# Kernel tuning notes

Measured on AMD Instinct MI355X. Metric: run time of the kernel, lower is better.

The kernel has to match this reference:

```python
import jax, jax.numpy as jnp
import numpy as np

OUT_FEATURES = 4096
IN_FEATURES = 4096
GROUP_SIZE = 256
NUM_GROUPS = OUT_FEATURES * IN_FEATURES // GROUP_SIZE  # 65536


def setup_inputs() -> dict:
    key = jax.random.key(0)
    k1, k2, k3 = jax.random.split(key, 3)
    x = jax.random.normal(k1, (4, 2048, IN_FEATURES), dtype=jnp.float32)
    weight_packed = jax.random.randint(k2, (NUM_GROUPS, GROUP_SIZE // 2), 0, 256, dtype=jnp.int32)
    # params[..., 0] = scale, params[..., 1] = zero_point; keep scales small like real quant params
    weight_params = jax.random.uniform(k3, (NUM_GROUPS, 2), dtype=jnp.float32) * jnp.array([0.01, 0.1], dtype=jnp.float32)
    return {"x": x, "weight_packed": weight_packed, "weight_params": weight_params}


def _dequantize_4bit(weight_packed, weight_params):
    # weight_packed: [G, gs/2] bytes, two 4-bit values per byte (low nibble = even index)
    scales = weight_params[:, 0:1]  # [G, 1]
    zeros = weight_params[:, 1:2]   # [G, 1]
    low = (weight_packed & 15).astype(jnp.float32)          # even positions
    high = ((weight_packed >> 4) & 15).astype(jnp.float32)  # odd positions
    q = jnp.stack([low, high], axis=-1).reshape(weight_packed.shape[0], -1)  # [G, gs]
    return q * scales + zeros


def reference(x, weight_packed, weight_params):
    w = _dequantize_4bit(weight_packed, weight_params)  # [G, gs]
    w = w.reshape(-1)[: OUT_FEATURES * IN_FEATURES].reshape(OUT_FEATURES, IN_FEATURES)
    # F.linear(x, W) = x @ W.T
    return jnp.einsum("bsi,oi->bso", x, w)
```

## Files before the change

### kernel.cpp

```cpp
#include <hip/hip_runtime.h>
#include <hip/hip_bf16.h>


#define M_DIM 8192
#define N_DIM 4096
#define K_DIM 4096

typedef __bf16 bf16x8 __attribute__((ext_vector_type(8)));
typedef float f32x4 __attribute__((ext_vector_type(4)));
typedef unsigned short us8 __attribute__((ext_vector_type(8)));

__device__ __forceinline__ unsigned short f2bf_rne(float f) {
    unsigned int u = __builtin_bit_cast(unsigned int, f);
    u += 0x7FFFu + ((u >> 16) & 1u);
    return (unsigned short)(u >> 16);
}

__global__ void prep_kernel(const float* __restrict__ x,
                            const int* __restrict__ packed,
                            const float* __restrict__ params,
                            ushort* __restrict__ a,
                            ushort* __restrict__ w) {
    int b = blockIdx.x;
    if (b < 16384) {
        int j = b * 256 + threadIdx.x;
        float4 v0 = ((const float4*)x)[2 * j];
        float4 v1 = ((const float4*)x)[2 * j + 1];
        us8 o;
        o[0] = f2bf_rne(v0.x); o[1] = f2bf_rne(v0.y);
        o[2] = f2bf_rne(v0.z); o[3] = f2bf_rne(v0.w);
        o[4] = f2bf_rne(v1.x); o[5] = f2bf_rne(v1.y);
        o[6] = f2bf_rne(v1.z); o[7] = f2bf_rne(v1.w);
        ((us8*)a)[j] = o;
    } else {
        int j = (b - 16384) * 256 + threadIdx.x;
        int4 v = ((const int4*)packed)[j];
        int g = j >> 5;
        float s = params[2 * g], z = params[2 * g + 1];
        unsigned int o0, o1, o2, o3;
        o0 = (unsigned int)f2bf_rne((float)(v.x & 15) * s + z)
           | ((unsigned int)f2bf_rne((float)((v.x >> 4) & 15) * s + z) << 16);
        o1 = (unsigned int)f2bf_rne((float)(v.y & 15) * s + z)
           | ((unsigned int)f2bf_rne((float)((v.y >> 4) & 15) * s + z) << 16);
        o2 = (unsigned int)f2bf_rne((float)(v.z & 15) * s + z)
           | ((unsigned int)f2bf_rne((float)((v.z >> 4) & 15) * s + z) << 16);
        o3 = (unsigned int)f2bf_rne((float)(v.w & 15) * s + z)
           | ((unsigned int)f2bf_rne((float)((v.w >> 4) & 15) * s + z) << 16);
        ((uint4*)w)[j] = make_uint4(o0, o1, o2, o3);
    }
}

__global__ __launch_bounds__(512, 2) void gemm_bt(const ushort* __restrict__ A,
                                                  const ushort* __restrict__ B,
                                                  float* __restrict__ C) {
    __shared__ ushort lds[65536];

    const int tid  = threadIdx.x;
    const int w    = tid >> 6;
    const int lane = tid & 63;
    const int quad = lane >> 4;
    const int l16  = lane & 15;
    const int wm   = w >> 2;
    const int wn   = w & 3;

    const int bid = blockIdx.x;
    const int sid = (bid & 7) * 64 + (bid >> 3);
    const int by  = sid & 31;
    const int bx  = sid >> 5;
    const int m0  = by * 256;
    const int n0  = bx * 256;

    const int srow = tid >> 3;
    const int scol = ((tid & 7) ^ (srow & 7)) * 8;
    const ushort* aS = A + (size_t)(m0 + srow) * K_DIM + scol;
    const ushort* bS = B + (size_t)(n0 + srow) * K_DIM + scol;

    f32x4 acc[8][4] = {};
    bf16x8 afA[2][2], afB[2][2];
    bf16x8 bf0a[4], bf0b[4];
    bf16x8 bf1[4];

    auto stageA = [&](int t, int h) {
        const int kc   = (t < 64 ? t : 63) * 64;
        const int slot = ((t & 1) * 2 + h) * 8192;
#pragma unroll
        for (int l = 0; l < 2; ++l)
            __builtin_amdgcn_global_load_lds(
                (const __attribute__((address_space(1))) void*)(aS + (size_t)(h * 128 + l * 64) * K_DIM + kc),
                (__attribute__((address_space(3))) void*)(lds + slot + (l * 512 + w * 64) * 8),
                16, 0, 0);
    };
    auto stageB = [&](int t, int h) {
        const int kc   = (t < 64 ? t : 63) * 64;
        const int slot = 32768 + ((t & 1) * 2 + h) * 8192;
#pragma unroll
        for (int l = 0; l < 2; ++l)
            __builtin_amdgcn_global_load_lds(
                (const __attribute__((address_space(1))) void*)(bS + (size_t)(h * 128 + l * 64) * K_DIM + kc),
                (__attribute__((address_space(3))) void*)(lds + slot + (l * 512 + w * 64) * 8),
                16, 0, 0);
    };

    const int aBase = wm * 8192;
    const int bBase = 32768 + (wn >> 1) * 8192;
    const int bR0   = (wn & 1) * 64;
    const int swz8  = l16 & 7;

    auto readAF = [&](bf16x8 (&dst)[2][2], int buf, int ph) {
#pragma unroll
        for (int ii = 0; ii < 2; ++ii)
#pragma unroll
            for (int ks = 0; ks < 2; ++ks)
                dst[ii][ks] = *(const bf16x8*)&lds[aBase + buf +
                    (ph * 32 + ii * 16 + l16) * 64 + ((ks * 4 + quad) ^ swz8) * 8];
    };
    auto readBF0 = [&](bf16x8 (&dst)[4], int buf) {
#pragma unroll
        for (int j = 0; j < 4; ++j)
            dst[j] = *(const bf16x8*)&lds[bBase + buf +
                (bR0 + j * 16 + l16) * 64 + (quad ^ swz8) * 8];
    };
    auto readBF1 = [&](int buf) {
#pragma unroll
        for (int j = 0; j < 4; ++j)
            bf1[j] = *(const bf16x8*)&lds[bBase + buf +
                (bR0 + j * 16 + l16) * 64 + ((4 + quad) ^ swz8) * 8];
    };

#define MFMA_PH(PH, AF, BF0)                                                   \
    do {                                                                       \
        __builtin_amdgcn_s_setprio(1);                                         \
        _Pragma("unroll")                                                      \
        for (int ii = 0; ii < 2; ++ii)                                         \
            _Pragma("unroll")                                                  \
            for (int j = 0; j < 4; ++j)                                        \
                acc[(PH) * 2 + ii][j] = __builtin_amdgcn_mfma_f32_16x16x32_bf16( \
                    AF[ii][0], BF0[j], acc[(PH) * 2 + ii][j], 0, 0, 0);        \
        _Pragma("unroll")                                                      \
        for (int ii = 0; ii < 2; ++ii)                                         \
            _Pragma("unroll")                                                  \
            for (int j = 0; j < 4; ++j)                                        \
                acc[(PH) * 2 + ii][j] = __builtin_amdgcn_mfma_f32_16x16x32_bf16( \
                    AF[ii][1], bf1[j], acc[(PH) * 2 + ii][j], 0, 0, 0);        \
        __builtin_amdgcn_s_setprio(0);                                         \
    } while (0)

    stageB(0, 0); stageB(0, 1); stageA(0, 0); stageA(0, 1); stageB(1, 0); stageB(1, 1);
    asm volatile("s_waitcnt vmcnt(4)" ::: "memory");
    __builtin_amdgcn_s_barrier();
    asm volatile("" ::: "memory");
    readBF0(bf0a, 0);
    readAF(afA, 0, 0);

#define TILE(T, BUF, NBUF, BF0C, BF0N)                                         \
    do {                                                                       \
        const int t = (T);                                                     \
                                                                      \
        readBF1(BUF);                                                          \
        readAF(afB, BUF, 1);                                                   \
        stageA(t + 1, 0);                                                      \
        MFMA_PH(0, afA, BF0C);                                                 \
                                                                      \
        readAF(afA, BUF, 2);                                                   \
        stageA(t + 1, 1);                                                      \
        MFMA_PH(1, afB, BF0C);                                                 \
        asm volatile("s_waitcnt lgkmcnt(0)" ::: "memory");                     \
        __builtin_amdgcn_sched_barrier(0);                                     \
        __builtin_amdgcn_s_barrier();                 \
        asm volatile("" ::: "memory");                                         \
                                                                      \
        readAF(afB, BUF, 3);                                                   \
        stageB(t + 2, 0);                                                      \
        MFMA_PH(2, afA, BF0C);                                                 \
                                                                      \
        stageB(t + 2, 1);                                                      \
        asm volatile("s_waitcnt vmcnt(4) lgkmcnt(0)" ::: "memory");            \
        __builtin_amdgcn_s_barrier();                \
        asm volatile("" ::: "memory");                                         \
        if (t < 63) { readBF0(BF0N, NBUF); readAF(afA, NBUF, 0); }             \
        __builtin_amdgcn_sched_barrier(0);                                     \
        MFMA_PH(3, afB, BF0C);                                                 \
    } while (0)

#pragma unroll 1
    for (int tt = 0; tt < 64; tt += 2) {
        TILE(tt,     0,     16384, bf0a, bf0b);
        TILE(tt + 1, 16384, 0,     bf0b, bf0a);
    }
#undef TILE
#undef MFMA_PH

    const int crow = m0 + wm * 128 + quad * 4;
    const int ccol = n0 + wn * 64 + l16;
#pragma unroll
    for (int rf = 0; rf < 8; ++rf)
#pragma unroll
        for (int j = 0; j < 4; ++j)
#pragma unroll
            for (int r = 0; r < 4; ++r)
                C[(size_t)(crow + rf * 16 + r) * N_DIM + ccol + j * 16] = acc[rf][j][r];
}

__global__ void naive_kernel(const float* __restrict__ x, const int* __restrict__ packed,
                             const float* __restrict__ params, float* __restrict__ out) {
    int idx = blockIdx.x * blockDim.x + threadIdx.x;
    if (idx >= M_DIM * N_DIM) return;
    int m = idx / N_DIM, o = idx % N_DIM;
    const float* xr = x + (size_t)m * K_DIM;
    float sum = 0.f;
    for (int gi = 0; gi < K_DIM / 256; ++gi) {
        int g = o * (K_DIM / 256) + gi;
        float s = params[2 * g], z = params[2 * g + 1];
        const int* p = packed + (size_t)g * 128;
        const float* xx = xr + gi * 256;
        for (int j = 0; j < 128; ++j) {
            int v = p[j];
            sum += xx[2 * j]     * ((float)(v & 15) * s + z);
            sum += xx[2 * j + 1] * ((float)((v >> 4) & 15) * s + z);
        }
    }
    out[idx] = sum;
}

extern "C" void kernel_launch(void* const* d_in, const int* in_sizes, int n_in,
                              void* d_out, int out_size, void* d_ws, size_t ws_size,
                              hipStream_t stream) {
    const float* x      = (const float*)d_in[0];
    const int*   packed = (const int*)d_in[1];
    const float* params = (const float*)d_in[2];
    float* out = (float*)d_out;

    const size_t a_bytes = (size_t)M_DIM * K_DIM * 2;
    const size_t w_bytes = (size_t)N_DIM * K_DIM * 2;

    if (ws_size >= a_bytes + w_bytes) {
        ushort* Abf = (ushort*)d_ws;
        ushort* Wbf = (ushort*)((char*)d_ws + a_bytes);

        prep_kernel<<<24576, 256, 0, stream>>>(x, packed, params, Abf, Wbf);

        gemm_bt<<<512, 512, 0, stream>>>(Abf, Wbf, out);
    } else {
        int n = M_DIM * N_DIM;
        naive_kernel<<<(n + 255) / 256, 256, 0, stream>>>(x, packed, params, out);
    }
}
```

Measured before the change: 445.2 us.

## Triple-buffer A fragments, precompute LDS read pointers, and remap block-to-XCD tiling

Adds a third A-fragment register set so the phase-2 A fragments are read from LDS at the start of each tile, alongside phase 1, instead of between MFMA phases. LDS read addresses now come from precomputed base pointers plus constant offsets, which cuts per-read address arithmetic. The block-to-tile mapping now gives each XCD a contiguous band of 4 M-rows across all 16 N-columns, aiming for better L2 reuse of B. The extra fragment registers raise pressure under launch_bounds(512,2) and could cause spills.

```diff
diff --git a/kernel.cpp b/kernel.cpp
--- a/kernel.cpp
+++ b/kernel.cpp
@@ -64,9 +64,10 @@
     const int wn   = w & 3;
 
     const int bid = blockIdx.x;
-    const int sid = (bid & 7) * 64 + (bid >> 3);
-    const int by  = sid & 31;
-    const int bx  = sid >> 5;
+    const int xcd = bid & 7;
+    const int idx = bid >> 3;
+    const int by  = xcd * 4 + (idx >> 4);
+    const int bx  = idx & 15;
     const int m0  = by * 256;
     const int n0  = bx * 256;
 
@@ -76,7 +77,7 @@
     const ushort* bS = B + (size_t)(n0 + srow) * K_DIM + scol;
 
     f32x4 acc[8][4] = {};
-    bf16x8 afA[2][2], afB[2][2];
+    bf16x8 afA0[2][2], afA1[2][2], afA2[2][2];
     bf16x8 bf0a[4], bf0b[4];
     bf16x8 bf1[4];
 
@@ -105,27 +106,12 @@
     const int bBase = 32768 + (wn >> 1) * 8192;
     const int bR0   = (wn & 1) * 64;
     const int swz8  = l16 & 7;
-
-    auto readAF = [&](bf16x8 (&dst)[2][2], int buf, int ph) {
-#pragma unroll
-        for (int ii = 0; ii < 2; ++ii)
-#pragma unroll
-            for (int ks = 0; ks < 2; ++ks)
-                dst[ii][ks] = *(const bf16x8*)&lds[aBase + buf +
-                    (ph * 32 + ii * 16 + l16) * 64 + ((ks * 4 + quad) ^ swz8) * 8];
-    };
-    auto readBF0 = [&](bf16x8 (&dst)[4], int buf) {
-#pragma unroll
-        for (int j = 0; j < 4; ++j)
-            dst[j] = *(const bf16x8*)&lds[bBase + buf +
-                (bR0 + j * 16 + l16) * 64 + (quad ^ swz8) * 8];
-    };
-    auto readBF1 = [&](int buf) {
-#pragma unroll
-        for (int j = 0; j < 4; ++j)
-            bf1[j] = *(const bf16x8*)&lds[bBase + buf +
-                (bR0 + j * 16 + l16) * 64 + ((4 + quad) ^ swz8) * 8];
-    };
+    const int c0    = (quad ^ swz8) * 8;
+    const int c1    = ((4 + quad) ^ swz8) * 8;
+    const ushort* pA0 = lds + aBase + l16 * 64 + c0;
+    const ushort* pA1 = lds + aBase + l16 * 64 + c1;
+    const ushort* pB0 = lds + bBase + (bR0 + l16) * 64 + c0;
+    const ushort* pB1 = lds + bBase + (bR0 + l16) * 64 + c1;
 
 #define MFMA_PH(PH, AF, BF0)                                                   \
     do {                                                                       \
@@ -145,41 +131,62 @@
         __builtin_amdgcn_s_setprio(0);                                         \
     } while (0)
 
+#define READ_A(DST, BUF, PH)                                                   \
+    do {                                                                       \
+        _Pragma("unroll")                                                      \
+        for (int ii = 0; ii < 2; ++ii) {                                       \
+            DST[ii][0] = *(const bf16x8*)(pA0 + (BUF) + ((PH) * 32 + ii * 16) * 64); \
+            DST[ii][1] = *(const bf16x8*)(pA1 + (BUF) + ((PH) * 32 + ii * 16) * 64); \
+        }                                                                      \
+    } while (0)
+#define READ_B0(DST, BUF)                                                      \
+    do {                                                                       \
+        _Pragma("unroll")                                                      \
+        for (int j = 0; j < 4; ++j)                                            \
+            DST[j] = *(const bf16x8*)(pB0 + (BUF) + j * 1024);                 \
+    } while (0)
+#define READ_B1(BUF)                                                           \
+    do {                                                                       \
+        _Pragma("unroll")                                                      \
+        for (int j = 0; j < 4; ++j)                                            \
+            bf1[j] = *(const bf16x8*)(pB1 + (BUF) + j * 1024);                 \
+    } while (0)
+
     stageB(0, 0); stageB(0, 1); stageA(0, 0); stageA(0, 1); stageB(1, 0); stageB(1, 1);
     asm volatile("s_waitcnt vmcnt(4)" ::: "memory");
     __builtin_amdgcn_s_barrier();
     asm volatile("" ::: "memory");
-    readBF0(bf0a, 0);
-    readAF(afA, 0, 0);
+    READ_B0(bf0a, 0);
+    READ_A(afA0, 0, 0);
 
 #define TILE(T, BUF, NBUF, BF0C, BF0N)                                         \
     do {                                                                       \
         const int t = (T);                                                     \
-                                                                      \
-        readBF1(BUF);                                                          \
-        readAF(afB, BUF, 1);                                                   \
+                                                    \
+        READ_B1(BUF);                                                          \
+        READ_A(afA1, BUF, 1);                                                  \
+        READ_A(afA2, BUF, 2);                                                  \
         stageA(t + 1, 0);                                                      \
-        MFMA_PH(0, afA, BF0C);                                                 \
-                                                                      \
-        readAF(afA, BUF, 2);                                                   \
+        MFMA_PH(0, afA0, BF0C);                                                \
+                                   \
         stageA(t + 1, 1);                                                      \
-        MFMA_PH(1, afB, BF0C);                                                 \
+        MFMA_PH(1, afA1, BF0C);                                                \
         asm volatile("s_waitcnt lgkmcnt(0)" ::: "memory");                     \
         __builtin_amdgcn_sched_barrier(0);                                     \
         __builtin_amdgcn_s_barrier();                 \
         asm volatile("" ::: "memory");                                         \
                                                                       \
-        readAF(afB, BUF, 3);                                                   \
+        READ_A(afA1, BUF, 3);                          \
         stageB(t + 2, 0);                                                      \
-        MFMA_PH(2, afA, BF0C);                                                 \
+        MFMA_PH(2, afA2, BF0C);                                                \
                                                                       \
         stageB(t + 2, 1);                                                      \
         asm volatile("s_waitcnt vmcnt(4) lgkmcnt(0)" ::: "memory");            \
         __builtin_amdgcn_s_barrier();                \
         asm volatile("" ::: "memory");                                         \
-        if (t < 63) { readBF0(BF0N, NBUF); readAF(afA, NBUF, 0); }             \
+        if (t < 63) { READ_B0(BF0N, NBUF); READ_A(afA0, NBUF, 0); }            \
         __builtin_amdgcn_sched_barrier(0);                                     \
-        MFMA_PH(3, afB, BF0C);                                                 \
+        MFMA_PH(3, afA1, BF0C);                                                \
     } while (0)
 
 #pragma unroll 1
@@ -189,6 +196,9 @@
     }
 #undef TILE
 #undef MFMA_PH
+#undef READ_A
+#undef READ_B0
+#undef READ_B1
 
     const int crow = m0 + wm * 128 + quad * 4;
     const int ccol = n0 + wn * 64 + l16;
```

New measurement: 469.0 us. 5.4% more time.
